# Performance work log

Hardware: AMD Instinct MI355X
Metric: run time of the kernel (lower is better)

The kernel has to match this reference:

```python
import jax, jax.numpy as jnp
import numpy as np

B, H, W, C = 32, 64, 64, 384
WS = 8            # window size (square)
NH = 12           # num heads
HD = C // NH      # head dim
SCALE = HD ** -0.5


def setup_inputs() -> dict:
    key = jax.random.key(0)
    ks = jax.random.split(key, 5)
    std = 0.02
    return {
        "x": jax.random.normal(ks[0], (B, H, W, C), dtype=jnp.float32),
        "w_qkv": jax.random.normal(ks[1], (C, 3 * C), dtype=jnp.float32) * std,
        "b_qkv": jnp.zeros((3 * C,), dtype=jnp.float32),
        "w_proj": jax.random.normal(ks[2], (C, C), dtype=jnp.float32) * std,
        "b_proj": jnp.zeros((C,), dtype=jnp.float32),
    }


def reference(x, w_qkv, b_qkv, w_proj, b_proj):
    b, h, w, c = x.shape
    nh_win, nw_win = h // WS, w // WS
    # window partition: (B, nh, WS, nw, WS, C) -> (B*nw_total, WS*WS, C)
    xw = x.reshape(b, nh_win, WS, nw_win, WS, c)
    xw = xw.transpose(0, 1, 3, 2, 4, 5).reshape(b * nh_win * nw_win, WS * WS, c)
    nW, T = xw.shape[0], WS * WS
    # qkv projection
    qkv = xw @ w_qkv + b_qkv                      # (nW, T, 3C)
    qkv = qkv.reshape(nW, T, 3, NH, HD).transpose(2, 0, 3, 1, 4)
    q, k, v = qkv[0], qkv[1], qkv[2]              # (nW, NH, T, HD)
    attn = jnp.einsum('wntd,wnsd->wnts', q, k) * SCALE
    attn = jax.nn.softmax(attn, axis=-1)
    out = jnp.einsum('wnts,wnsd->wntd', attn, v)  # (nW, NH, T, HD)
    out = out.transpose(0, 2, 1, 3).reshape(nW, T, c)
    out = out @ w_proj + b_proj
    # window reverse
    out = out.reshape(b, nh_win, nw_win, WS, WS, c)
    out = out.transpose(0, 1, 3, 2, 4, 5).reshape(b, h, w, c)
    return out
```

## Files before the change

### kernel.cpp

```cpp
#include <hip/hip_runtime.h>
#include <hip/hip_bf16.h>

typedef __bf16 bfv8 __attribute__((ext_vector_type(8)));
typedef float f32x4 __attribute__((ext_vector_type(4)));
typedef unsigned int u32;

#define MFMA(a,b,c) __builtin_amdgcn_mfma_f32_16x16x32_bf16((a),(b),(c),0,0,0)

constexpr int XW_LD = 392;

__global__ __launch_bounds__(256)
void prep_weights(const float* __restrict__ w_qkv, const float* __restrict__ w_proj,
                  unsigned short* __restrict__ qT, unsigned short* __restrict__ pT)
{
    int i = blockIdx.x * 256 + threadIdx.x;
    const int NQ = 1152 * 384;
    if (i < NQ) {
        int c = i / 384, k = i - c * 384;
        __bf16 h = (__bf16)w_qkv[k * 1152 + c];
        qT[i] = *(unsigned short*)&h;
    } else {
        int j = i - NQ;
        if (j < 384 * 384) {
            int c = j / 384, k = j - c * 384;
            __bf16 h = (__bf16)w_proj[k * 384 + c];
            pT[j] = *(unsigned short*)&h;
        }
    }
}

__device__ __forceinline__ u32 pkbf(float a, float b) {
    __bf16 x = (__bf16)a, y = (__bf16)b;
    unsigned short lo = *(unsigned short*)&x, hi = *(unsigned short*)&y;
    return ((u32)hi << 16) | lo;
}

__device__ __forceinline__ bfv8 conv_frag(u32 p00, u32 p01, u32 p10, u32 p11,
                                          int abase, bool selhi)
{
    union { u32 u[4]; bfv8 v; } cv;
    #pragma unroll
    for (int w = 0; w < 4; ++w) {
        const int addr = abase + (w >> 1) * 64;
        const int lo_ = __builtin_amdgcn_ds_bpermute(addr, (int)((w & 1) ? p01 : p00));
        const int hi_ = __builtin_amdgcn_ds_bpermute(addr, (int)((w & 1) ? p11 : p10));
        cv.u[w] = (u32)(selhi ? hi_ : lo_);
    }
    return cv.v;
}

__global__ __launch_bounds__(256, 3)
void win_attn(const float* __restrict__ x,
              const float* __restrict__ b_qkv,
              const float* __restrict__ b_proj,
              const unsigned short* __restrict__ qT_,
              const unsigned short* __restrict__ pT_,
              float* __restrict__ out)
{
    __shared__ __bf16 sX[64 * XW_LD];

    const __bf16* wqkvT  = (const __bf16*)qT_;
    const __bf16* wprojT = (const __bf16*)pT_;

    const int wid  = blockIdx.x;
    const int bb   = wid >> 6;
    const int wy   = (wid >> 3) & 7;
    const int wx   = wid & 7;
    const int tid  = threadIdx.x;
    const int lane = tid & 63;
    const int wv   = tid >> 6;
    const int lr   = lane & 15;
    const int lg   = lane >> 4;
    const int k8   = lg * 8;

    const size_t gbase = ((size_t)(bb * 64 + wy * 8) * 64 + wx * 8) * 384;

    {
        const float* xb = x + gbase;
        for (int i = tid; i < 64 * 96; i += 256) {
            int t  = i / 96;
            int c4 = (i - t * 96) * 4;
            const float4 v = *(const float4*)(xb + (size_t)((t >> 3) * 64 + (t & 7)) * 384 + c4);
            *(uint2*)&sX[t * XW_LD + c4] = make_uint2(pkbf(v.x, v.y), pkbf(v.z, v.w));
        }
    }
    __syncthreads();

    const int   abase = ((lg & 1) * 32 + lr) * 4;
    const bool  selhi = (lg & 2) != 0;
    const float SC    = 0.17677669529663687f;

    u32 opk[3][4][2][2];

    #pragma unroll
    for (int hl = 0; hl < 3; ++hl) {
        const int h  = wv * 3 + hl;
        const int cQ = h * 32, cK = cQ + 384, cV = cQ + 768;

        f32x4 aq[2][4], ak[2][4], av[4][2];
        #pragma unroll
        for (int a = 0; a < 2; ++a)
            #pragma unroll
            for (int b = 0; b < 4; ++b) { aq[a][b] = f32x4{0,0,0,0}; ak[a][b] = f32x4{0,0,0,0}; av[b][a] = f32x4{0,0,0,0}; }

        const __bf16* wqp = wqkvT + (size_t)(cQ + lr) * 384 + k8;
        const __bf16* wkp = wqkvT + (size_t)(cK + lr) * 384 + k8;
        const __bf16* wvp = wqkvT + (size_t)(cV + lr) * 384 + k8;
        const __bf16* xp  = &sX[lr * XW_LD + k8];

        #pragma unroll 2
        for (int kk = 0; kk < 12; ++kk) {
            bfv8 xf[4], wqf[2], wkf[2], wvf[2];
            #pragma unroll
            for (int t4 = 0; t4 < 4; ++t4) xf[t4] = *(const bfv8*)(xp + t4 * 16 * XW_LD + kk * 32);
            #pragma unroll
            for (int hdt = 0; hdt < 2; ++hdt) {
                wqf[hdt] = *(const bfv8*)(wqp + (size_t)hdt * 16 * 384 + kk * 32);
                wkf[hdt] = *(const bfv8*)(wkp + (size_t)hdt * 16 * 384 + kk * 32);
                wvf[hdt] = *(const bfv8*)(wvp + (size_t)hdt * 16 * 384 + kk * 32);
            }
            #pragma unroll
            for (int hdt = 0; hdt < 2; ++hdt)
                #pragma unroll
                for (int t4 = 0; t4 < 4; ++t4) {
                    aq[hdt][t4] = MFMA(wqf[hdt], xf[t4], aq[hdt][t4]);
                    ak[hdt][t4] = MFMA(wkf[hdt], xf[t4], ak[hdt][t4]);
                    av[t4][hdt] = MFMA(xf[t4], wvf[hdt], av[t4][hdt]);
                }
        }

        float bqv[2][4], bkv[2][4], bvv[2];
        #pragma unroll
        for (int hdt = 0; hdt < 2; ++hdt) {
            #pragma unroll
            for (int r = 0; r < 4; ++r) {
                bqv[hdt][r] = b_qkv[cQ + hdt * 16 + lg * 4 + r];
                bkv[hdt][r] = b_qkv[cK + hdt * 16 + lg * 4 + r];
            }
            bvv[hdt] = b_qkv[cV + hdt * 16 + lr];
        }

        u32 pkQ[2][4][2], pkK[2][4][2], pkV[4][2][2];
        #pragma unroll
        for (int hdt = 0; hdt < 2; ++hdt)
            #pragma unroll
            for (int t4 = 0; t4 < 4; ++t4)
                #pragma unroll
                for (int p = 0; p < 2; ++p) {
                    pkQ[hdt][t4][p] = pkbf((aq[hdt][t4][2 * p] + bqv[hdt][2 * p]) * SC,
                                           (aq[hdt][t4][2 * p + 1] + bqv[hdt][2 * p + 1]) * SC);
                    pkK[hdt][t4][p] = pkbf(ak[hdt][t4][2 * p] + bkv[hdt][2 * p],
                                           ak[hdt][t4][2 * p + 1] + bkv[hdt][2 * p + 1]);
                    pkV[t4][hdt][p] = pkbf(av[t4][hdt][2 * p] + bvv[hdt],
                                           av[t4][hdt][2 * p + 1] + bvv[hdt]);
                }

        bfv8 Qf[4];
        #pragma unroll
        for (int qt = 0; qt < 4; ++qt)
            Qf[qt] = conv_frag(pkQ[0][qt][0], pkQ[0][qt][1], pkQ[1][qt][0], pkQ[1][qt][1], abase, selhi);
        f32x4 st[4][4];
        #pragma unroll
        for (int kt = 0; kt < 4; ++kt) {
            const bfv8 kf = conv_frag(pkK[0][kt][0], pkK[0][kt][1], pkK[1][kt][0], pkK[1][kt][1], abase, selhi);
            #pragma unroll
            for (int qt = 0; qt < 4; ++qt) {
                f32x4 z{};
                st[kt][qt] = MFMA(kf, Qf[qt], z);
            }
        }

        float rinv[4];
        #pragma unroll
        for (int qt = 0; qt < 4; ++qt) {
            float mx = -1e30f;
            #pragma unroll
            for (int kt = 0; kt < 4; ++kt)
                #pragma unroll
                for (int r = 0; r < 4; ++r) mx = fmaxf(mx, st[kt][qt][r]);
            mx = fmaxf(mx, __shfl_xor(mx, 16, 64));
            mx = fmaxf(mx, __shfl_xor(mx, 32, 64));
            float sum = 0.f;
            #pragma unroll
            for (int kt = 0; kt < 4; ++kt)
                #pragma unroll
                for (int r = 0; r < 4; ++r) { st[kt][qt][r] = __expf(st[kt][qt][r] - mx); sum += st[kt][qt][r]; }
            sum += __shfl_xor(sum, 16, 64);
            sum += __shfl_xor(sum, 32, 64);
            rinv[qt] = 1.f / sum;
        }
        u32 pkP[4][4][2];
        #pragma unroll
        for (int qt = 0; qt < 4; ++qt)
            #pragma unroll
            for (int kt = 0; kt < 4; ++kt)
                #pragma unroll
                for (int p = 0; p < 2; ++p)
                    pkP[qt][kt][p] = pkbf(st[kt][qt][2 * p] * rinv[qt], st[kt][qt][2 * p + 1] * rinv[qt]);

        bfv8 Vf[2][2];
        #pragma unroll
        for (int ks = 0; ks < 2; ++ks)
            #pragma unroll
            for (int hdt = 0; hdt < 2; ++hdt)
                Vf[ks][hdt] = conv_frag(pkV[2 * ks][hdt][0], pkV[2 * ks][hdt][1],
                                        pkV[2 * ks + 1][hdt][0], pkV[2 * ks + 1][hdt][1], abase, selhi);
        f32x4 o[4][2];
        #pragma unroll
        for (int qt = 0; qt < 4; ++qt)
            #pragma unroll
            for (int hdt = 0; hdt < 2; ++hdt) o[qt][hdt] = f32x4{0,0,0,0};
        #pragma unroll
        for (int qt = 0; qt < 4; ++qt)
            #pragma unroll
            for (int ks = 0; ks < 2; ++ks) {
                const bfv8 pf = conv_frag(pkP[qt][2 * ks][0], pkP[qt][2 * ks][1],
                                          pkP[qt][2 * ks + 1][0], pkP[qt][2 * ks + 1][1], abase, selhi);
                #pragma unroll
                for (int hdt = 0; hdt < 2; ++hdt)
                    o[qt][hdt] = MFMA(pf, Vf[ks][hdt], o[qt][hdt]);
            }
        #pragma unroll
        for (int qt = 0; qt < 4; ++qt)
            #pragma unroll
            for (int hdt = 0; hdt < 2; ++hdt)
                #pragma unroll
                for (int p = 0; p < 2; ++p)
                    opk[hl][qt][hdt][p] = pkbf(o[qt][hdt][2 * p], o[qt][hdt][2 * p + 1]);
    }

    __syncthreads();

    #pragma unroll
    for (int hl = 0; hl < 3; ++hl)
        #pragma unroll
        for (int qt = 0; qt < 4; ++qt)
            #pragma unroll
            for (int hdt = 0; hdt < 2; ++hdt)
                #pragma unroll
                for (int p = 0; p < 2; ++p) {
                    const u32 u = opk[hl][qt][hdt][p];
                    const int row0 = qt * 16 + lg * 4 + 2 * p;
                    const int col  = (wv * 3 + hl) * 32 + hdt * 16 + lr;
                    unsigned short lo = (unsigned short)(u & 0xffff);
                    unsigned short hi = (unsigned short)(u >> 16);
                    sX[row0 * XW_LD + col]       = *(__bf16*)&lo;
                    sX[(row0 + 1) * XW_LD + col] = *(__bf16*)&hi;
                }
    __syncthreads();

    {
        const int nb = wv * 96;
        const __bf16* bp = wprojT + (size_t)(nb + lr) * 384 + k8;
        f32x4 acc[4][6];
        #pragma unroll
        for (int m = 0; m < 4; ++m)
            #pragma unroll
            for (int nt = 0; nt < 6; ++nt) acc[m][nt] = f32x4{0,0,0,0};
        #pragma unroll 2
        for (int kk = 0; kk < 12; ++kk) {
            bfv8 bfr[6];
            #pragma unroll
            for (int nt = 0; nt < 6; ++nt)
                bfr[nt] = *(const bfv8*)(bp + (size_t)nt * 16 * 384 + kk * 32);
            #pragma unroll
            for (int m = 0; m < 4; ++m) {
                const bfv8 af = *(const bfv8*)&sX[(m * 16 + lr) * XW_LD + kk * 32 + k8];
                #pragma unroll
                for (int nt = 0; nt < 6; ++nt)
                    acc[m][nt] = MFMA(af, bfr[nt], acc[m][nt]);
            }
        }
        float bpj[6];
        #pragma unroll
        for (int nt = 0; nt < 6; ++nt) bpj[nt] = b_proj[nb + nt * 16 + lr];
        float* ob = out + gbase;
        #pragma unroll
        for (int m = 0; m < 4; ++m)
            #pragma unroll
            for (int r = 0; r < 4; ++r) {
                const int t = m * 16 + lg * 4 + r;
                float* op = ob + (size_t)((t >> 3) * 64 + (t & 7)) * 384 + nb;
                #pragma unroll
                for (int nt = 0; nt < 6; ++nt)
                    op[nt * 16 + lr] = acc[m][nt][r] + bpj[nt];
            }
    }
}

extern "C" void kernel_launch(void* const* d_in, const int* in_sizes, int n_in,
                              void* d_out, int out_size, void* d_ws, size_t ws_size,
                              hipStream_t stream)
{
    const float* x      = (const float*)d_in[0];
    const float* w_qkv  = (const float*)d_in[1];
    const float* b_qkv  = (const float*)d_in[2];
    const float* w_proj = (const float*)d_in[3];
    const float* b_proj = (const float*)d_in[4];
    float* out = (float*)d_out;

    unsigned short* qT = (unsigned short*)d_ws;
    unsigned short* pT = qT + 1152 * 384;

    const int NPREP = 1152 * 384 + 384 * 384;
    prep_weights<<<(NPREP + 255) / 256, 256, 0, stream>>>(w_qkv, w_proj, qT, pT);
    win_attn<<<2048, 256, 0, stream>>>(x, b_qkv, b_proj, qT, pT, out);
}
```

Before: 412.7 us.

## Stage projection output through LDS for float4 stores; add MFMA priority hints

The projection epilogue now writes accumulators into shared memory in two 32-row halves, then stores them to global memory as coalesced float4 rows. This replaces scattered 4-byte per-lane stores. The change also wraps the MFMA loops in s_setprio raise/lower calls and stops unrolling the per-head loop, which may cut register pressure. In exchange it adds extra barriers and an LDS round trip, and the rolled head loop may block some cross-iteration scheduling.

After: 382.2 us. 1.08x faster.

```diff
diff --git a/kernel.cpp b/kernel.cpp
--- a/kernel.cpp
+++ b/kernel.cpp
@@ -92,7 +92,7 @@
 
     u32 opk[3][4][2][2];
 
-    #pragma unroll
+    #pragma unroll 1
     for (int hl = 0; hl < 3; ++hl) {
         const int h  = wv * 3 + hl;
         const int cQ = h * 32, cK = cQ + 384, cV = cQ + 768;
@@ -108,6 +108,7 @@
         const __bf16* wvp = wqkvT + (size_t)(cV + lr) * 384 + k8;
         const __bf16* xp  = &sX[lr * XW_LD + k8];
 
+        __builtin_amdgcn_s_setprio(1);
         #pragma unroll 2
         for (int kk = 0; kk < 12; ++kk) {
             bfv8 xf[4], wqf[2], wkf[2], wvf[2];
@@ -128,6 +129,7 @@
                     av[t4][hdt] = MFMA(xf[t4], wvf[hdt], av[t4][hdt]);
                 }
         }
+        __builtin_amdgcn_s_setprio(0);
 
         float bqv[2][4], bkv[2][4], bvv[2];
         #pragma unroll
@@ -160,6 +162,7 @@
         for (int qt = 0; qt < 4; ++qt)
             Qf[qt] = conv_frag(pkQ[0][qt][0], pkQ[0][qt][1], pkQ[1][qt][0], pkQ[1][qt][1], abase, selhi);
         f32x4 st[4][4];
+        __builtin_amdgcn_s_setprio(1);
         #pragma unroll
         for (int kt = 0; kt < 4; ++kt) {
             const bfv8 kf = conv_frag(pkK[0][kt][0], pkK[0][kt][1], pkK[1][kt][0], pkK[1][kt][1], abase, selhi);
@@ -169,6 +172,7 @@
                 st[kt][qt] = MFMA(kf, Qf[qt], z);
             }
         }
+        __builtin_amdgcn_s_setprio(0);
 
         float rinv[4];
         #pragma unroll
@@ -210,6 +214,7 @@
         for (int qt = 0; qt < 4; ++qt)
             #pragma unroll
             for (int hdt = 0; hdt < 2; ++hdt) o[qt][hdt] = f32x4{0,0,0,0};
+        __builtin_amdgcn_s_setprio(1);
         #pragma unroll
         for (int qt = 0; qt < 4; ++qt)
             #pragma unroll
@@ -220,6 +225,7 @@
                 for (int hdt = 0; hdt < 2; ++hdt)
                     o[qt][hdt] = MFMA(pf, Vf[ks][hdt], o[qt][hdt]);
             }
+        __builtin_amdgcn_s_setprio(0);
         #pragma unroll
         for (int qt = 0; qt < 4; ++qt)
             #pragma unroll
@@ -249,14 +255,15 @@
                 }
     __syncthreads();
 
+    const int nb = wv * 96;
+    f32x4 acc[4][6];
     {
-        const int nb = wv * 96;
         const __bf16* bp = wprojT + (size_t)(nb + lr) * 384 + k8;
-        f32x4 acc[4][6];
         #pragma unroll
         for (int m = 0; m < 4; ++m)
             #pragma unroll
             for (int nt = 0; nt < 6; ++nt) acc[m][nt] = f32x4{0,0,0,0};
+        __builtin_amdgcn_s_setprio(1);
         #pragma unroll 2
         for (int kk = 0; kk < 12; ++kk) {
             bfv8 bfr[6];
@@ -271,20 +278,37 @@
                     acc[m][nt] = MFMA(af, bfr[nt], acc[m][nt]);
             }
         }
-        float bpj[6];
-        #pragma unroll
-        for (int nt = 0; nt < 6; ++nt) bpj[nt] = b_proj[nb + nt * 16 + lr];
-        float* ob = out + gbase;
-        #pragma unroll
-        for (int m = 0; m < 4; ++m)
+        __builtin_amdgcn_s_setprio(0);
+    }
+    float bpj[6];
+    #pragma unroll
+    for (int nt = 0; nt < 6; ++nt) bpj[nt] = b_proj[nb + nt * 16 + lr];
+
+    __syncthreads();
+    float* sF = (float*)sX;
+    float* ob = out + gbase;
+    #pragma unroll
+    for (int half = 0; half < 2; ++half) {
+        #pragma unroll
+        for (int mm = 0; mm < 2; ++mm) {
+            const int m = half * 2 + mm;
             #pragma unroll
             for (int r = 0; r < 4; ++r) {
-                const int t = m * 16 + lg * 4 + r;
-                float* op = ob + (size_t)((t >> 3) * 64 + (t & 7)) * 384 + nb;
+                const int row = mm * 16 + lg * 4 + r;
                 #pragma unroll
                 for (int nt = 0; nt < 6; ++nt)
-                    op[nt * 16 + lr] = acc[m][nt][r] + bpj[nt];
-            }
+                    sF[row * 384 + nb + nt * 16 + lr] = acc[m][nt][r] + bpj[nt];
+            }
+        }
+        __syncthreads();
+        for (int i = tid; i < 32 * 96; i += 256) {
+            const int row = i / 96;
+            const int c4  = (i - row * 96) * 4;
+            const int t   = half * 32 + row;
+            const float4 v = *(const float4*)&sF[row * 384 + c4];
+            *(float4*)(ob + (size_t)((t >> 3) * 64 + (t & 7)) * 384 + c4) = v;
+        }
+        if (half == 0) __syncthreads();
     }
 }
 
```
